# Kernel optimization log

Measured on AMD Instinct MI355X. Metric: run time of the kernel, lower is better.

Reference implementation:

```python
import jax, jax.numpy as jnp
import numpy as np

T, B, F = 512, 512, 14
H1, H2 = 32, 64


def setup_inputs() -> dict:
    key = jax.random.key(0)
    ks = jax.random.split(key, 16)
    s1 = 1.0 / np.sqrt(H1)
    s2 = 1.0 / np.sqrt(H2)
    u = lambda k, shape, s: jax.random.uniform(k, shape, jnp.float32, -s, s)
    return {
        "x": jax.random.normal(ks[0], (T, B, F), jnp.float32),
        # LSTM layer 1 (PyTorch gate order i,f,g,o)
        "W_ih1": u(ks[1], (4 * H1, F), s1),
        "W_hh1": u(ks[2], (4 * H1, H1), s1),
        "b_ih1": u(ks[3], (4 * H1,), s1),
        "b_hh1": u(ks[4], (4 * H1,), s1),
        # LSTM layer 2
        "W_ih2": u(ks[5], (4 * H2, H1), s2),
        "W_hh2": u(ks[6], (4 * H2, H2), s2),
        "b_ih2": u(ks[7], (4 * H2,), s2),
        "b_hh2": u(ks[8], (4 * H2,), s2),
        # MLP head
        "W_fc1": u(ks[9], (8, H2), 1.0 / np.sqrt(H2)),
        "b_fc1": u(ks[10], (8,), 1.0 / np.sqrt(H2)),
        "W_fc2": u(ks[11], (8, 8), 1.0 / np.sqrt(8)),
        "b_fc2": u(ks[12], (8,), 1.0 / np.sqrt(8)),
        "W_fc": u(ks[13], (1, 8), 1.0 / np.sqrt(8)),
        "b_fc": u(ks[14], (1,), 1.0 / np.sqrt(8)),
    }


def _gates(g, c):
    # PyTorch LSTM gate order: input, forget, cell(g), output
    i, f, gg, o = jnp.split(g, 4, axis=-1)
    c_new = jax.nn.sigmoid(f) * c + jax.nn.sigmoid(i) * jnp.tanh(gg)
    h_new = jax.nn.sigmoid(o) * jnp.tanh(c_new)
    return h_new, c_new


def reference(x, W_ih1, W_hh1, b_ih1, b_hh1, W_ih2, W_hh2, b_ih2, b_hh2,
              W_fc1, b_fc1, W_fc2, b_fc2, W_fc, b_fc):
    Bv = x.shape[1]
    # Fold the input projection of layer 1 outside the scan (one big GEMM).
    xg = jnp.einsum('tbf,gf->tbg', x, W_ih1) + b_ih1 + b_hh1  # [T,B,4H1]

    def step(carry, xg_t):
        h1, c1, h2 = carry
        h1, c1 = _gates(xg_t + h1 @ W_hh1.T, c1)
        # Layer 2: original code never carries c_t2 -> incoming cell is always 0.
        g2 = h1 @ W_ih2.T + b_ih2 + h2 @ W_hh2.T + b_hh2
        h2, _ = _gates(g2, jnp.zeros((Bv, H2), x.dtype))
        return (h1, c1, h2), None

    init = (jnp.zeros((Bv, H1), x.dtype),
            jnp.zeros((Bv, H1), x.dtype),
            jnp.zeros((Bv, H2), x.dtype))
    (h1, c1, h2), _ = jax.lax.scan(step, init, xg)

    out = jax.nn.relu(h2)
    out = jax.nn.relu(out @ W_fc1.T + b_fc1)
    out = jax.nn.relu(out @ W_fc2.T + b_fc2)
    return out @ W_fc.T + b_fc  # [B,1]
```

## Files before the change

kernel.cpp:

```cpp
#include <hip/hip_runtime.h>
#include <math.h>

#define TT 512
#define BB 512
#define FF 14
#define H1 32
#define H2 64
#define NR 8
#define NBLK (BB / NR)

typedef _Float16 half8   __attribute__((ext_vector_type(8)));
typedef _Float16 half4_t __attribute__((ext_vector_type(4)));
typedef float    float4v __attribute__((ext_vector_type(4)));

typedef __attribute__((address_space(1))) const half4_t g_half4;

#if __has_builtin(__builtin_amdgcn_exp2f)
__device__ __forceinline__ float exp2_(float x) { return __builtin_amdgcn_exp2f(x); }
#else
__device__ __forceinline__ float exp2_(float x) { return exp2f(x); }
#endif
__device__ __forceinline__ float rcpf_(float x) { return __builtin_amdgcn_rcpf(x); }

__device__ __forceinline__ float dpp_ror8_(float v) {
    return __int_as_float(__builtin_amdgcn_update_dpp(
        0, __float_as_int(v), 0x128 , 0xF, 0xF, true));
}

#define K1L 1.4426950408889634f
#define K2L 2.8853901617779268f

__device__ __forceinline__ float4v mfma16(half8 a, half8 b, float4v c) {
    return __builtin_amdgcn_mfma_f32_16x16x32_f16(a, b, c, 0, 0, 0);
}

__device__ __forceinline__ int bfrag_off(int k, int n) {
    const int slab = k >> 5, k5 = k & 31;
    const int dl = n + 16 * ((k5 >> 3) & 3);
    const int dw = (k5 >> 1) & 3;
    return ((slab * 256 + dl * 4 + dw) << 1) | (k5 & 1);
}

__global__ __launch_bounds__(512)
void xg_precompute(const float* __restrict__ x,
                   const float* __restrict__ Wih1,
                   const float* __restrict__ bih1,
                   const float* __restrict__ bhh1,
                   _Float16* __restrict__ xg)
{
    const int t    = blockIdx.x >> 3;
    const int seg  = blockIdx.x & 7;
    const int l    = threadIdx.x;
    const int lane = l & 63;
    const int w    = l >> 6;
    const int n    = lane & 15;
    const int quad = lane >> 4;
    const int u1   = w * 4 + quad;

    float wr[4][FF];
    float bs[4];
    #pragma unroll
    for (int r = 0; r < 4; ++r) {
        const int row = r * 32 + u1;
        #pragma unroll
        for (int f = 0; f < FF; ++f) wr[r][f] = Wih1[row * FF + f];
        bs[r] = bih1[row] + bhh1[row];
    }

    half4_t* og = (half4_t*)xg + (size_t)t * (NBLK * 256);
    #pragma unroll 2
    for (int bi = 0; bi < 8; ++bi) {
        const int blk = seg * 8 + bi;
        const int row = blk * NR + (n & 7);
        const float* xp = x + ((size_t)t * BB + row) * FF;
        float xv[FF];
        #pragma unroll
        for (int e = 0; e < 7; ++e) {
            const float2 v = *(const float2*)(xp + 2 * e);
            xv[2 * e] = v.x; xv[2 * e + 1] = v.y;
        }
        half4_t o16;
        #pragma unroll
        for (int r = 0; r < 4; ++r) {
            float a = bs[r];
            #pragma unroll
            for (int f = 0; f < FF; ++f) a = fmaf(xv[f], wr[r][f], a);
            o16[r] = (_Float16)a;
        }
        if (n < 8) og[blk * 256 + w * 32 + quad * 8 + n] = o16;
    }
}

#define XGOFF(t_) ((size_t)(t_) * (NBLK * 256))

__global__ __launch_bounds__(512)
__attribute__((amdgpu_waves_per_eu(2, 2)))
void lstm3_v21(
    const _Float16* __restrict__ xg,
    const float* __restrict__ Wih2, const float* __restrict__ Whh1,
    const float* __restrict__ Whh2,
    const float* __restrict__ bih2, const float* __restrict__ bhh2,
    const float* __restrict__ Wfc1, const float* __restrict__ bfc1,
    const float* __restrict__ Wfc2, const float* __restrict__ bfc2,
    const float* __restrict__ Wfc,  const float* __restrict__ bfc,
    float* __restrict__ out)
{
    const int row0 = blockIdx.x * NR;
    const int l    = threadIdx.x;
    const int lane = l & 63;
    const int w    = l >> 6;
    const int n    = lane & 15;
    const int quad = lane >> 4;
    const int hi   = n >> 3;

    __shared__ __align__(16) unsigned s2f[2][3 * 256];
    __shared__ _Float16 h2plain[NR][H2];
    __shared__ float mlp1[NR][8];
    __shared__ float mlp2[NR][8];

    half8 a2[2][3];
    float4v bias2[2];
    #pragma unroll
    for (int tt = 0; tt < 2; ++tt) {
        const int T = 2 * w + tt;
        const int m = T * 16 + n;
        const int row = (m & 3) * 64 + (m >> 2);
        #pragma unroll
        for (int s = 0; s < 3; ++s) {
            const int k0 = s * 32 + quad * 8;
            half8 a;
            if (k0 < H1) {
                #pragma unroll
                for (int j = 0; j < 8; ++j) a[j] = (_Float16)Wih2[row * H1 + k0 + j];
            } else {
                #pragma unroll
                for (int j = 0; j < 8; ++j) a[j] = (_Float16)Whh2[row * H2 + (k0 - H1) + j];
            }
            a2[tt][s] = a;
        }
        const int u = T * 4 + quad;
        #pragma unroll
        for (int r = 0; r < 4; ++r) {
            const int br = r * 64 + u;
            bias2[tt][r] = bih2[br] + bhh2[br];
        }
    }

    half8 a1h;
    {
        const int m = w * 16 + n;
        const int row = (m & 3) * 32 + (m >> 2);
        #pragma unroll
        for (int j = 0; j < 8; ++j)
            a1h[j] = (_Float16)Whh1[row * H1 + quad * 8 + j];
    }

    const int u1    = w * 4 + quad;
    const int offB  = bfrag_off(u1, n);
    const int u2sel = (2 * w + hi) * 4 + quad;
    const int off2n = bfrag_off(32 + u2sel, n & 7);

    const g_half4* xgb = (const g_half4*)((const half4_t*)xg
                        + (size_t)blockIdx.x * 256 + (w * 32 + quad * 8 + (n & 7)));

    float c1r = 0.0f;

    for (int z = l; z < 2 * 3 * 256; z += 512) ((unsigned*)s2f)[z] = 0u;

    half4_t xg0 = xgb[XGOFF(0)];
    half4_t xgA = xgb[XGOFF(1)];
    half4_t xgB = xgb[XGOFF(2)];
    half4_t xgC = xgb[XGOFF(3)];
    half4_t xgD = xgb[XGOFF(4)];
    __syncthreads();

#define LSTM_STEP(i_, CP_, RP_, XG_) do {                                          \
        const half8 tb0 = *(const half8*)(s2f[RP_] + lane * 4);                    \
        const half8 tb1 = *(const half8*)(s2f[RP_] + 256 + lane * 4);              \
        const half8 tb2 = *(const half8*)(s2f[RP_] + 512 + lane * 4);              \
        const half4_t xh = XG_;             \
        { int tn_ = (i_) + 4; if (tn_ > TT - 1) tn_ = TT - 1;                      \
          XG_ = xgb[XGOFF(tn_)]; }                                                 \
        float4v cin_;                                                              \
        cin_[0] = (float)xh[0]; cin_[1] = (float)xh[1];                            \
        cin_[2] = (float)xh[2]; cin_[3] = (float)xh[3];                            \
        float4v acc1 = mfma16(a1h, tb0, cin_);                                     \
        {   const float Ei = exp2_(-K1L * acc1[0]);                                \
            const float Ef = exp2_(-K1L * acc1[1]);                                \
            const float Eg = exp2_(-K2L * acc1[2]);                                \
            const float Eo = exp2_(-K1L * acc1[3]);                                \
            const float P  = (1.0f + Ei) * (1.0f + Eg);                            \
            const float pf = 1.0f + Ef;                                            \
            const float cn = fmaf(c1r, P, pf * (1.0f - Eg)) * rcpf_(pf * P);       \
            c1r = cn;                                                              \
            const float Ec = exp2_(-K2L * cn);                                     \
            const float hh = (1.0f - Ec) * rcpf_((1.0f + Eo) * (1.0f + Ec));       \
            ((_Float16*)s2f[CP_])[offB] = (_Float16)hh; }                          \
        float4v p0 = bias2[0];                                                     \
        p0 = mfma16(a2[0][0], tb0, p0);                                            \
        p0 = mfma16(a2[0][1], tb1, p0);                                            \
        p0 = mfma16(a2[0][2], tb2, p0);                                            \
        float4v p1 = bias2[1];                                                     \
        p1 = mfma16(a2[1][0], tb0, p1);                                            \
        p1 = mfma16(a2[1][1], tb1, p1);                                            \
        p1 = mfma16(a2[1][2], tb2, p1);                                            \
        float4v ps;                                                                \
        _Pragma("unroll")                                                          \
        for (int r = 0; r < 4; ++r) {                                              \
            const float sw = dpp_ror8_(p1[r]);                                     \
            ps[r] = hi ? sw : p0[r];                                               \
        }                                                                          \
        {   const float Ei = exp2_(-K1L * ps[0]);                                  \
            const float Eg = exp2_(-K2L * ps[2]);                                  \
            const float Eo = exp2_(-K1L * ps[3]);                                  \
            const float c2 = (1.0f - Eg) * rcpf_((1.0f + Ei) * (1.0f + Eg));       \
            const float Ec = exp2_(-K2L * c2);                                     \
            const float h  = (1.0f - Ec) * rcpf_((1.0f + Eo) * (1.0f + Ec));       \
            ((_Float16*)s2f[CP_])[off2n] = (_Float16)h; }                          \
        asm volatile("s_waitcnt lgkmcnt(0)" ::: "memory");                         \
        __builtin_amdgcn_s_barrier();                                              \
        asm volatile("" ::: "memory");                                             \
    } while (0)

    {
        const float gi = (float)xg0[0], gg = (float)xg0[2], go = (float)xg0[3];
        const float Ei = exp2_(-K1L * gi);
        const float Eg = exp2_(-K2L * gg);
        const float Eo = exp2_(-K1L * go);
        const float cn = (1.0f - Eg) * rcpf_((1.0f + Ei) * (1.0f + Eg));
        c1r = cn;
        const float Ec = exp2_(-K2L * cn);
        const float hh = (1.0f - Ec) * rcpf_((1.0f + Eo) * (1.0f + Ec));
        ((_Float16*)s2f[0])[offB] = (_Float16)hh;
        asm volatile("s_waitcnt lgkmcnt(0)" ::: "memory");
        __builtin_amdgcn_s_barrier();
        asm volatile("" ::: "memory");
    }

    #pragma unroll 1
    for (int ii = 0; ii < 127; ++ii) {
        const int i0 = 4 * ii + 1;
        LSTM_STEP(i0,     1, 0, xgA);
        LSTM_STEP(i0 + 1, 0, 1, xgB);
        LSTM_STEP(i0 + 2, 1, 0, xgC);
        LSTM_STEP(i0 + 3, 0, 1, xgD);
    }
    LSTM_STEP(509, 1, 0, xgA);
    LSTM_STEP(510, 0, 1, xgB);
    LSTM_STEP(511, 1, 0, xgC);

    {
        const half8 tb0 = *(const half8*)(s2f[1] + lane * 4);
        const half8 tb1 = *(const half8*)(s2f[1] + 256 + lane * 4);
        const half8 tb2 = *(const half8*)(s2f[1] + 512 + lane * 4);
        float4v p0 = bias2[0];
        p0 = mfma16(a2[0][0], tb0, p0);
        p0 = mfma16(a2[0][1], tb1, p0);
        p0 = mfma16(a2[0][2], tb2, p0);
        float4v p1 = bias2[1];
        p1 = mfma16(a2[1][0], tb0, p1);
        p1 = mfma16(a2[1][1], tb1, p1);
        p1 = mfma16(a2[1][2], tb2, p1);
        float4v ps;
        #pragma unroll
        for (int r = 0; r < 4; ++r) {
            const float sw = dpp_ror8_(p1[r]);
            ps[r] = hi ? sw : p0[r];
        }
        const float Ei = exp2_(-K1L * ps[0]);
        const float Eg = exp2_(-K2L * ps[2]);
        const float Eo = exp2_(-K1L * ps[3]);
        const float c2 = (1.0f - Eg) * rcpf_((1.0f + Ei) * (1.0f + Eg));
        const float Ec = exp2_(-K2L * c2);
        const float h  = (1.0f - Ec) * rcpf_((1.0f + Eo) * (1.0f + Ec));
        h2plain[n & 7][u2sel] = (_Float16)h;
        __syncthreads();
    }

    if (l < NR * 8) {
        const int rr = l >> 3, j = l & 7;
        float a = bfc1[j];
        #pragma unroll
        for (int k = 0; k < H2; ++k)
            a = fmaf(fmaxf((float)h2plain[rr][k], 0.0f), Wfc1[j * H2 + k], a);
        mlp1[rr][j] = fmaxf(a, 0.0f);
    }
    __syncthreads();
    if (l < NR * 8) {
        const int rr = l >> 3, j = l & 7;
        float a = bfc2[j];
        #pragma unroll
        for (int k = 0; k < 8; ++k) a = fmaf(mlp1[rr][k], Wfc2[j * 8 + k], a);
        mlp2[rr][j] = fmaxf(a, 0.0f);
    }
    __syncthreads();
    if (l < NR) {
        float a = bfc[0];
        #pragma unroll
        for (int k = 0; k < 8; ++k) a = fmaf(mlp2[l][k], Wfc[k], a);
        out[row0 + l] = a;
    }
#undef LSTM_STEP
}

__device__ __forceinline__ float sigmoidf_(float x) { return rcpf_(1.0f + __expf(-x)); }
__device__ __forceinline__ float tanhf_(float x) {
    float e = __expf(-2.0f * fabsf(x));
    float t = (1.0f - e) * rcpf_(1.0f + e);
    return copysignf(t, x);
}

__global__ __launch_bounds__(512)
__attribute__((amdgpu_waves_per_eu(2, 2)))
void lstm3_kernel(
    const float* __restrict__ x,
    const float* __restrict__ Wih1, const float* __restrict__ Whh1,
    const float* __restrict__ bih1, const float* __restrict__ bhh1,
    const float* __restrict__ Wih2, const float* __restrict__ Whh2,
    const float* __restrict__ bih2, const float* __restrict__ bhh2,
    const float* __restrict__ Wfc1, const float* __restrict__ bfc1,
    const float* __restrict__ Wfc2, const float* __restrict__ bfc2,
    const float* __restrict__ Wfc,  const float* __restrict__ bfc,
    float* __restrict__ out)
{
    const int row0 = blockIdx.x * 16;
    const int l    = threadIdx.x;
    const int lane = l & 63;
    const int w    = l >> 6;
    const int n    = lane & 15;
    const int quad = lane >> 4;

    __shared__ __align__(16) unsigned s2f[2][3 * 256];
    __shared__ _Float16 h2plain[16][H2];
    __shared__ float mlp1[16][8];
    __shared__ float mlp2[16][8];

    half8 a2[2][3];
    float4v bias2[2];
    #pragma unroll
    for (int tt = 0; tt < 2; ++tt) {
        const int T = 2 * w + tt;
        const int m = T * 16 + n;
        const int row = (m & 3) * 64 + (m >> 2);
        #pragma unroll
        for (int s = 0; s < 3; ++s) {
            const int k0 = s * 32 + quad * 8;
            half8 a;
            if (k0 < H1) {
                #pragma unroll
                for (int j = 0; j < 8; ++j) a[j] = (_Float16)Wih2[row * H1 + k0 + j];
            } else {
                #pragma unroll
                for (int j = 0; j < 8; ++j) a[j] = (_Float16)Whh2[row * H2 + (k0 - H1) + j];
            }
            a2[tt][s] = a;
        }
        const int u = T * 4 + quad;
        #pragma unroll
        for (int r = 0; r < 4; ++r) {
            const int br = r * 64 + u;
            bias2[tt][r] = bih2[br] + bhh2[br];
        }
    }

    half8 a1x, a1h;
    float4v bias1;
    {
        const int m = w * 16 + n;
        const int row = (m & 3) * 32 + (m >> 2);
        #pragma unroll
        for (int j = 0; j < 8; ++j) {
            const int k = quad * 8 + j;
            a1x[j] = (_Float16)((k < FF) ? Wih1[row * FF + k] : 0.0f);
            a1h[j] = (_Float16)Whh1[row * H1 + k];
        }
        const int u1_ = w * 4 + quad;
        #pragma unroll
        for (int r = 0; r < 4; ++r) {
            const int br = r * 32 + u1_;
            bias1[r] = bih1[br] + bhh1[br];
        }
    }

    const int u1   = w * 4 + quad;
    const int offB = bfrag_off(u1, n);
    int off2[2];
    #pragma unroll
    for (int tt = 0; tt < 2; ++tt)
        off2[tt] = bfrag_off(32 + (2 * w + tt) * 4 + quad, n);

    const int b1q  = quad & 1;
    const int xrow = (row0 + n) * FF;
    const int xo0 = 8 * b1q;
    const int xo1 = 8 * b1q + 2;
    const int xo2 = 8 * b1q + 4;
    const int xo3 = 6 * b1q + 6;

    float c1r = 0.0f;
    float2 xr0[4], xr1[4];

    for (int z = l; z < 2 * 3 * 256; z += 512) ((unsigned*)s2f)[z] = 0u;

    {
        const float* xp = x + xrow;
        xr0[0] = *(const float2*)(xp + xo0);
        xr0[1] = *(const float2*)(xp + xo1);
        xr0[2] = *(const float2*)(xp + xo2);
        xr0[3] = *(const float2*)(xp + xo3);
        const float* xq = x + BB * FF + xrow;
        xr1[0] = *(const float2*)(xq + xo0);
        xr1[1] = *(const float2*)(xq + xo1);
        xr1[2] = *(const float2*)(xq + xo2);
        xr1[3] = *(const float2*)(xq + xo3);
    }
    __syncthreads();

#define LSTM_STEP_F(i_, CP_, RP_, XR_) do {                                        \
        const half8 tb0 = *(const half8*)(s2f[RP_] + lane * 4);                    \
        const half8 tb1 = *(const half8*)(s2f[RP_] + 256 + lane * 4);              \
        const half8 tb2 = *(const half8*)(s2f[RP_] + 512 + lane * 4);              \
        half8 xb;                                                                  \
        xb[0] = (_Float16)XR_[0].x; xb[1] = (_Float16)XR_[0].y;                    \
        xb[2] = (_Float16)XR_[1].x; xb[3] = (_Float16)XR_[1].y;                    \
        xb[4] = (_Float16)XR_[2].x; xb[5] = (_Float16)XR_[2].y;                    \
        xb[6] = (_Float16)XR_[3].x; xb[7] = (_Float16)XR_[3].y;                    \
        { int tn_ = (i_) + 2; if (tn_ > TT - 1) tn_ = TT - 1;                      \
          const float* xp_ = x + tn_ * (BB * FF) + xrow;                           \
          XR_[0] = *(const float2*)(xp_ + xo0);                                    \
          XR_[1] = *(const float2*)(xp_ + xo1);                                    \
          XR_[2] = *(const float2*)(xp_ + xo2);                                    \
          XR_[3] = *(const float2*)(xp_ + xo3); }                                  \
        float4v acc1 = mfma16(a1x, xb, bias1);                                     \
        acc1 = mfma16(a1h, tb0, acc1);                                             \
        const float cn1 = sigmoidf_(acc1[1]) * c1r                                 \
                        + sigmoidf_(acc1[0]) * tanhf_(acc1[2]);                    \
        c1r = cn1;                                                                 \
        ((_Float16*)s2f[CP_])[offB] = (_Float16)(sigmoidf_(acc1[3]) * tanhf_(cn1));\
        _Pragma("unroll")                                                          \
        for (int tt = 0; tt < 2; ++tt) {                                           \
            float4v acc = bias2[tt];                                               \
            acc = mfma16(a2[tt][0], tb0, acc);                                     \
            acc = mfma16(a2[tt][1], tb1, acc);                                     \
            acc = mfma16(a2[tt][2], tb2, acc);                                     \
            const float cn = sigmoidf_(acc[0]) * tanhf_(acc[2]);                   \
            const float h  = sigmoidf_(acc[3]) * tanhf_(cn);                       \
            ((_Float16*)s2f[CP_])[off2[tt]] = (_Float16)h;                         \
        }                                                                          \
        asm volatile("s_waitcnt lgkmcnt(0)" ::: "memory");                         \
        __builtin_amdgcn_s_barrier();                                              \
        asm volatile("" ::: "memory");                                             \
    } while (0)

    {
        half8 xb;
        xb[0] = (_Float16)xr0[0].x; xb[1] = (_Float16)xr0[0].y;
        xb[2] = (_Float16)xr0[1].x; xb[3] = (_Float16)xr0[1].y;
        xb[4] = (_Float16)xr0[2].x; xb[5] = (_Float16)xr0[2].y;
        xb[6] = (_Float16)xr0[3].x; xb[7] = (_Float16)xr0[3].y;
        {   const float* xp_ = x + 2 * (BB * FF) + xrow;
            xr0[0] = *(const float2*)(xp_ + xo0);
            xr0[1] = *(const float2*)(xp_ + xo1);
            xr0[2] = *(const float2*)(xp_ + xo2);
            xr0[3] = *(const float2*)(xp_ + xo3); }
        float4v acc1 = mfma16(a1x, xb, bias1);
        const float cn1 = sigmoidf_(acc1[0]) * tanhf_(acc1[2]);
        c1r = cn1;
        ((_Float16*)s2f[0])[offB] = (_Float16)(sigmoidf_(acc1[3]) * tanhf_(cn1));
        asm volatile("s_waitcnt lgkmcnt(0)" ::: "memory");
        __builtin_amdgcn_s_barrier();
        asm volatile("" ::: "memory");
    }

    #pragma unroll 1
    for (int ii = 0; ii < 255; ++ii) {
        const int i0 = 2 * ii + 1;
        LSTM_STEP_F(i0,     1, 0, xr1);
        LSTM_STEP_F(i0 + 1, 0, 1, xr0);
    }
    LSTM_STEP_F(511, 1, 0, xr1);

    {
        const half8 tb0 = *(const half8*)(s2f[1] + lane * 4);
        const half8 tb1 = *(const half8*)(s2f[1] + 256 + lane * 4);
        const half8 tb2 = *(const half8*)(s2f[1] + 512 + lane * 4);
        #pragma unroll
        for (int tt = 0; tt < 2; ++tt) {
            float4v acc = bias2[tt];
            acc = mfma16(a2[tt][0], tb0, acc);
            acc = mfma16(a2[tt][1], tb1, acc);
            acc = mfma16(a2[tt][2], tb2, acc);
            const float cn = sigmoidf_(acc[0]) * tanhf_(acc[2]);
            const float h  = sigmoidf_(acc[3]) * tanhf_(cn);
            h2plain[n][(2 * w + tt) * 4 + quad] = (_Float16)h;
        }
        __syncthreads();
    }

    if (l < 16 * 8) {
        const int rr = l >> 3, j = l & 7;
        float a = bfc1[j];
        #pragma unroll
        for (int k = 0; k < H2; ++k)
            a = fmaf(fmaxf((float)h2plain[rr][k], 0.0f), Wfc1[j * H2 + k], a);
        mlp1[rr][j] = fmaxf(a, 0.0f);
    }
    __syncthreads();
    if (l < 16 * 8) {
        const int rr = l >> 3, j = l & 7;
        float a = bfc2[j];
        #pragma unroll
        for (int k = 0; k < 8; ++k) a = fmaf(mlp1[rr][k], Wfc2[j * 8 + k], a);
        mlp2[rr][j] = fmaxf(a, 0.0f);
    }
    __syncthreads();
    if (l < 16) {
        float a = bfc[0];
        #pragma unroll
        for (int k = 0; k < 8; ++k) a = fmaf(mlp2[l][k], Wfc[k], a);
        out[row0 + l] = a;
    }
#undef LSTM_STEP_F
}

extern "C" void kernel_launch(void* const* d_in, const int* in_sizes, int n_in,
                              void* d_out, int out_size, void* d_ws, size_t ws_size,
                              hipStream_t stream) {
    const float* x    = (const float*)d_in[0];
    const float* Wih1 = (const float*)d_in[1];
    const float* Whh1 = (const float*)d_in[2];
    const float* bih1 = (const float*)d_in[3];
    const float* bhh1 = (const float*)d_in[4];
    const float* Wih2 = (const float*)d_in[5];
    const float* Whh2 = (const float*)d_in[6];
    const float* bih2 = (const float*)d_in[7];
    const float* bhh2 = (const float*)d_in[8];
    const float* Wfc1 = (const float*)d_in[9];
    const float* bfc1 = (const float*)d_in[10];
    const float* Wfc2 = (const float*)d_in[11];
    const float* bfc2 = (const float*)d_in[12];
    const float* Wfc  = (const float*)d_in[13];
    const float* bfc  = (const float*)d_in[14];
    float* out = (float*)d_out;

    const size_t xg_bytes = (size_t)TT * NBLK * 256 * sizeof(half4_t);
    if (d_ws != nullptr && ws_size >= xg_bytes) {
        _Float16* xg = (_Float16*)d_ws;
        xg_precompute<<<dim3(TT * 8), dim3(512), 0, stream>>>(x, Wih1, bih1, bhh1, xg);
        lstm3_v21<<<dim3(NBLK), dim3(512), 0, stream>>>(
            xg, Wih2, Whh1, Whh2, bih2, bhh2,
            Wfc1, bfc1, Wfc2, bfc2, Wfc, bfc, out);
    } else {
        lstm3_kernel<<<dim3(BB / 16), dim3(512), 0, stream>>>(
            x, Wih1, Whh1, bih1, bhh1, Wih2, Whh2, bih2, bhh2,
            Wfc1, bfc1, Wfc2, bfc2, Wfc, bfc, out);
    }
}
```

Before: 356.4 us.

## Split layer-1 and layer-2 LSTM work onto separate wave groups

Doubles the block to 1024 threads so waves 0-7 compute only layer 1 and waves 8-15 compute only layer 2 of the same timestep, sharing state through the double-buffered LDS tiles. This is meant to run the two layers' MFMA and transcendental chains in parallel on different waves instead of serially within each wave, which should shorten the per-step critical path. In exchange it doubles the number of waves taking part in every per-step barrier, and the per-wave register budget shrinks under waves_per_eu 4.

```diff
diff --git a/kernel.cpp b/kernel.cpp
--- a/kernel.cpp
+++ b/kernel.cpp
@@ -93,9 +93,9 @@
 
 #define XGOFF(t_) ((size_t)(t_) * (NBLK * 256))
 
-__global__ __launch_bounds__(512)
-__attribute__((amdgpu_waves_per_eu(2, 2)))
-void lstm3_v21(
+__global__ __launch_bounds__(1024)
+__attribute__((amdgpu_waves_per_eu(4, 4)))
+void lstm3_v22(
     const _Float16* __restrict__ xg,
     const float* __restrict__ Wih2, const float* __restrict__ Whh1,
     const float* __restrict__ Whh2,
@@ -108,7 +108,9 @@
     const int row0 = blockIdx.x * NR;
     const int l    = threadIdx.x;
     const int lane = l & 63;
-    const int w    = l >> 6;
+    const int wv   = l >> 6;
+    const int w    = wv & 7;
+    const bool isL1 = (wv < 8);
     const int n    = lane & 15;
     const int quad = lane >> 4;
     const int hi   = n >> 3;
@@ -120,34 +122,36 @@
 
     half8 a2[2][3];
     float4v bias2[2];
-    #pragma unroll
-    for (int tt = 0; tt < 2; ++tt) {
-        const int T = 2 * w + tt;
-        const int m = T * 16 + n;
-        const int row = (m & 3) * 64 + (m >> 2);
-        #pragma unroll
-        for (int s = 0; s < 3; ++s) {
-            const int k0 = s * 32 + quad * 8;
-            half8 a;
-            if (k0 < H1) {
-                #pragma unroll
-                for (int j = 0; j < 8; ++j) a[j] = (_Float16)Wih2[row * H1 + k0 + j];
-            } else {
-                #pragma unroll
-                for (int j = 0; j < 8; ++j) a[j] = (_Float16)Whh2[row * H2 + (k0 - H1) + j];
+    if (!isL1) {
+        #pragma unroll
+        for (int tt = 0; tt < 2; ++tt) {
+            const int T = 2 * w + tt;
+            const int m = T * 16 + n;
+            const int row = (m & 3) * 64 + (m >> 2);
+            #pragma unroll
+            for (int s = 0; s < 3; ++s) {
+                const int k0 = s * 32 + quad * 8;
+                half8 a;
+                if (k0 < H1) {
+                    #pragma unroll
+                    for (int j = 0; j < 8; ++j) a[j] = (_Float16)Wih2[row * H1 + k0 + j];
+                } else {
+                    #pragma unroll
+                    for (int j = 0; j < 8; ++j) a[j] = (_Float16)Whh2[row * H2 + (k0 - H1) + j];
+                }
+                a2[tt][s] = a;
             }
-            a2[tt][s] = a;
-        }
-        const int u = T * 4 + quad;
-        #pragma unroll
-        for (int r = 0; r < 4; ++r) {
-            const int br = r * 64 + u;
-            bias2[tt][r] = bih2[br] + bhh2[br];
+            const int u = T * 4 + quad;
+            #pragma unroll
+            for (int r = 0; r < 4; ++r) {
+                const int br = r * 64 + u;
+                bias2[tt][r] = bih2[br] + bhh2[br];
+            }
         }
     }
 
     half8 a1h;
-    {
+    if (isL1) {
         const int m = w * 16 + n;
         const int row = (m & 3) * 32 + (m >> 2);
         #pragma unroll
@@ -165,27 +169,30 @@
 
     float c1r = 0.0f;
 
-    for (int z = l; z < 2 * 3 * 256; z += 512) ((unsigned*)s2f)[z] = 0u;
-
-    half4_t xg0 = xgb[XGOFF(0)];
-    half4_t xgA = xgb[XGOFF(1)];
-    half4_t xgB = xgb[XGOFF(2)];
-    half4_t xgC = xgb[XGOFF(3)];
-    half4_t xgD = xgb[XGOFF(4)];
+    for (int z = l; z < 2 * 3 * 256; z += 1024) ((unsigned*)s2f)[z] = 0u;
+
+    half4_t xg0 = {0,0,0,0}, xgA = {0,0,0,0}, xgB = {0,0,0,0},
+            xgC = {0,0,0,0}, xgD = {0,0,0,0};
+    if (isL1) {
+        xg0 = xgb[XGOFF(0)];
+        xgA = xgb[XGOFF(1)];
+        xgB = xgb[XGOFF(2)];
+        xgC = xgb[XGOFF(3)];
+        xgD = xgb[XGOFF(4)];
+    }
     __syncthreads();
 
 #define LSTM_STEP(i_, CP_, RP_, XG_) do {                                          \
-        const half8 tb0 = *(const half8*)(s2f[RP_] + lane * 4);                    \
-        const half8 tb1 = *(const half8*)(s2f[RP_] + 256 + lane * 4);              \
-        const half8 tb2 = *(const half8*)(s2f[RP_] + 512 + lane * 4);              \
-        const half4_t xh = XG_;             \
-        { int tn_ = (i_) + 4; if (tn_ > TT - 1) tn_ = TT - 1;                      \
-          XG_ = xgb[XGOFF(tn_)]; }                                                 \
-        float4v cin_;                                                              \
-        cin_[0] = (float)xh[0]; cin_[1] = (float)xh[1];                            \
-        cin_[2] = (float)xh[2]; cin_[3] = (float)xh[3];                            \
-        float4v acc1 = mfma16(a1h, tb0, cin_);                                     \
-        {   const float Ei = exp2_(-K1L * acc1[0]);                                \
+        if (isL1) {                                                                \
+            const half8 tb0 = *(const half8*)(s2f[RP_] + lane * 4);                \
+            const half4_t xh = XG_;                                                \
+            { int tn_ = (i_) + 4; if (tn_ > TT - 1) tn_ = TT - 1;                  \
+              XG_ = xgb[XGOFF(tn_)]; }                                             \
+            float4v cin_;                                                          \
+            cin_[0] = (float)xh[0]; cin_[1] = (float)xh[1];                        \
+            cin_[2] = (float)xh[2]; cin_[3] = (float)xh[3];                        \
+            float4v acc1 = mfma16(a1h, tb0, cin_);                                 \
+            const float Ei = exp2_(-K1L * acc1[0]);                                \
             const float Ef = exp2_(-K1L * acc1[1]);                                \
             const float Eg = exp2_(-K2L * acc1[2]);                                \
             const float Eo = exp2_(-K1L * acc1[3]);                                \
@@ -195,43 +202,50 @@
             c1r = cn;                                                              \
             const float Ec = exp2_(-K2L * cn);                                     \
             const float hh = (1.0f - Ec) * rcpf_((1.0f + Eo) * (1.0f + Ec));       \
-            ((_Float16*)s2f[CP_])[offB] = (_Float16)hh; }                          \
-        float4v p0 = bias2[0];                                                     \
-        p0 = mfma16(a2[0][0], tb0, p0);                                            \
-        p0 = mfma16(a2[0][1], tb1, p0);                                            \
-        p0 = mfma16(a2[0][2], tb2, p0);                                            \
-        float4v p1 = bias2[1];                                                     \
-        p1 = mfma16(a2[1][0], tb0, p1);                                            \
-        p1 = mfma16(a2[1][1], tb1, p1);                                            \
-        p1 = mfma16(a2[1][2], tb2, p1);                                            \
-        float4v ps;                                                                \
-        _Pragma("unroll")                                                          \
-        for (int r = 0; r < 4; ++r) {                                              \
-            const float sw = dpp_ror8_(p1[r]);                                     \
-            ps[r] = hi ? sw : p0[r];                                               \
-        }                                                                          \
-        {   const float Ei = exp2_(-K1L * ps[0]);                                  \
+            ((_Float16*)s2f[CP_])[offB] = (_Float16)hh;                            \
+        } else {                                                                   \
+            const half8 tb0 = *(const half8*)(s2f[RP_] + lane * 4);                \
+            const half8 tb1 = *(const half8*)(s2f[RP_] + 256 + lane * 4);          \
+            const half8 tb2 = *(const half8*)(s2f[RP_] + 512 + lane * 4);          \
+            float4v p0 = bias2[0];                                                 \
+            p0 = mfma16(a2[0][0], tb0, p0);                                        \
+            p0 = mfma16(a2[0][1], tb1, p0);                                        \
+            p0 = mfma16(a2[0][2], tb2, p0);                                        \
+            float4v p1 = bias2[1];                                                 \
+            p1 = mfma16(a2[1][0], tb0, p1);                                        \
+            p1 = mfma16(a2[1][1], tb1, p1);                                        \
+            p1 = mfma16(a2[1][2], tb2, p1);                                        \
+            float4v ps;                                                            \
+            _Pragma("unroll")                                                      \
+            for (int r = 0; r < 4; ++r) {                                          \
+                const float sw = dpp_ror8_(p1[r]);                                 \
+                ps[r] = hi ? sw : p0[r];                                           \
+            }                                                                      \
+            const float Ei = exp2_(-K1L * ps[0]);                                  \
             const float Eg = exp2_(-K2L * ps[2]);                                  \
             const float Eo = exp2_(-K1L * ps[3]);                                  \
             const float c2 = (1.0f - Eg) * rcpf_((1.0f + Ei) * (1.0f + Eg));       \
             const float Ec = exp2_(-K2L * c2);                                     \
             const float h  = (1.0f - Ec) * rcpf_((1.0f + Eo) * (1.0f + Ec));       \
-            ((_Float16*)s2f[CP_])[off2n] = (_Float16)h; }                          \
+            ((_Float16*)s2f[CP_])[off2n] = (_Float16)h;                            \
+        }                                                                          \
         asm volatile("s_waitcnt lgkmcnt(0)" ::: "memory");                         \
         __builtin_amdgcn_s_barrier();                                              \
         asm volatile("" ::: "memory");                                             \
     } while (0)
 
     {
-        const float gi = (float)xg0[0], gg = (float)xg0[2], go = (float)xg0[3];
-        const float Ei = exp2_(-K1L * gi);
-        const float Eg = exp2_(-K2L * gg);
-        const float Eo = exp2_(-K1L * go);
-        const float cn = (1.0f - Eg) * rcpf_((1.0f + Ei) * (1.0f + Eg));
-        c1r = cn;
-        const float Ec = exp2_(-K2L * cn);
-        const float hh = (1.0f - Ec) * rcpf_((1.0f + Eo) * (1.0f + Ec));
-        ((_Float16*)s2f[0])[offB] = (_Float16)hh;
+        if (isL1) {
+            const float gi = (float)xg0[0], gg = (float)xg0[2], go = (float)xg0[3];
+            const float Ei = exp2_(-K1L * gi);
+            const float Eg = exp2_(-K2L * gg);
+            const float Eo = exp2_(-K1L * go);
+            const float cn = (1.0f - Eg) * rcpf_((1.0f + Ei) * (1.0f + Eg));
+            c1r = cn;
+            const float Ec = exp2_(-K2L * cn);
+            const float hh = (1.0f - Ec) * rcpf_((1.0f + Eo) * (1.0f + Ec));
+            ((_Float16*)s2f[0])[offB] = (_Float16)hh;
+        }
         asm volatile("s_waitcnt lgkmcnt(0)" ::: "memory");
         __builtin_amdgcn_s_barrier();
         asm volatile("" ::: "memory");
@@ -249,7 +263,7 @@
     LSTM_STEP(510, 0, 1, xgB);
     LSTM_STEP(511, 1, 0, xgC);
 
-    {
+    if (!isL1) {
         const half8 tb0 = *(const half8*)(s2f[1] + lane * 4);
         const half8 tb1 = *(const half8*)(s2f[1] + 256 + lane * 4);
         const half8 tb2 = *(const half8*)(s2f[1] + 512 + lane * 4);
@@ -274,8 +288,8 @@
         const float Ec = exp2_(-K2L * c2);
         const float h  = (1.0f - Ec) * rcpf_((1.0f + Eo) * (1.0f + Ec));
         h2plain[n & 7][u2sel] = (_Float16)h;
-        __syncthreads();
-    }
+    }
+    __syncthreads();
 
     if (l < NR * 8) {
         const int rr = l >> 3, j = l & 7;
@@ -546,7 +560,7 @@
     if (d_ws != nullptr && ws_size >= xg_bytes) {
         _Float16* xg = (_Float16*)d_ws;
         xg_precompute<<<dim3(TT * 8), dim3(512), 0, stream>>>(x, Wih1, bih1, bhh1, xg);
-        lstm3_v21<<<dim3(NBLK), dim3(512), 0, stream>>>(
+        lstm3_v22<<<dim3(NBLK), dim3(1024), 0, stream>>>(
             xg, Wih2, Whh1, Whh2, bih2, bhh2,
             Wfc1, bfc1, Wfc2, bfc2, Wfc, bfc, out);
     } else {
```

Result: faster. 344.3 us (-3.4%).
